# Optimization experiments

Measured on AMD Instinct MI355X. Metric: run time of the kernel, lower is better.

## Reference

```python
import jax, jax.numpy as jnp
import numpy as np

EPS = 1e-12  # F.normalize default eps

def _l1_normalize(x, axis):
    return x / jnp.maximum(jnp.sum(jnp.abs(x), axis=axis, keepdims=True), EPS)


def setup_inputs() -> dict:
    key = jax.random.key(0)
    k1, k2, k3, k4 = jax.random.split(key, 4)
    B_src, S_src, d = 4096, 32, 512
    B_tgt, T = 32, 256
    m = jax.random.normal(k1, (B_src, S_src, d), dtype=jnp.float32)
    om = jax.random.normal(k2, (B_tgt, T, d), dtype=jnp.float32)
    src_mask = jax.random.randint(k3, (B_src, 1, S_src), 0, 2, dtype=jnp.int32)
    tgt_mask = jax.random.randint(k4, (B_tgt, T, T), 0, 2, dtype=jnp.int32)
    return {"m": m, "om": om, "src_mask": src_mask, "tgt_mask": tgt_mask}


def reference(m, om, src_mask, tgt_mask):
    # masked mean readouts (L1-normalized masks as attention weights)
    src_w = _l1_normalize(src_mask.astype(jnp.float32), axis=-1)      # [B_src,1,S_src]
    src_readout = jnp.einsum('bos,bsd->bod', src_w, m)[:, 0, :]       # [B_src,d]
    tgt_w = _l1_normalize(tgt_mask.astype(jnp.float32), axis=-1)      # [B_tgt,T,T]
    tgt_readout = jnp.einsum('btu,bud->btd', tgt_w, om)               # [B_tgt,T,d]

    # pairwise L2 distance over d WITHOUT materializing [B_tgt,T,B_src,d]:
    # ||t - s||^2 = ||t||^2 + ||s||^2 - 2 t.s
    t_sq = jnp.sum(tgt_readout * tgt_readout, axis=-1)                # [B_tgt,T]
    s_sq = jnp.sum(src_readout * src_readout, axis=-1)                # [B_src]
    cross = jnp.einsum('btd,nd->btn', tgt_readout, src_readout)       # [B_tgt,T,B_src]
    d2 = t_sq[..., None] + s_sq[None, None, :] - 2.0 * cross
    dist = jnp.sqrt(jnp.maximum(d2, EPS))
    sim = jnp.exp(-dist)
    sim = _l1_normalize(sim, axis=-1)                                 # [B_tgt,T,B_src]
    return sim
```

## Files before the change

kernel.cpp:

```cpp
#include <hip/hip_runtime.h>
#include <math.h>

#define EPSF 1e-12f

typedef short bf16x8 __attribute__((ext_vector_type(8)));
typedef float f32x4 __attribute__((ext_vector_type(4)));

__device__ __forceinline__ void gload_lds16(const void* g, void* l) {
  __builtin_amdgcn_global_load_lds(
      (const __attribute__((address_space(1))) unsigned int*)g,
      (__attribute__((address_space(3))) unsigned int*)l, 16, 0, 0);
}

__device__ __forceinline__ unsigned short bf16_rne(float f) {
  unsigned int u = __float_as_uint(f);
  u += 0x7fffu + ((u >> 16) & 1u);
  return (unsigned short)(u >> 16);
}

__device__ __forceinline__ float bf16_to_f32(unsigned short h) {
  return __uint_as_float((unsigned int)h << 16);
}

__device__ __forceinline__ float block_reduce_sum_256(float v) {
#pragma unroll
  for (int o = 32; o > 0; o >>= 1) v += __shfl_down(v, o, 64);
  __shared__ float ws4[4];
  const int lane = threadIdx.x & 63;
  const int w = threadIdx.x >> 6;
  if (lane == 0) ws4[w] = v;
  __syncthreads();
  if (threadIdx.x == 0) ws4[0] = ws4[0] + ws4[1] + ws4[2] + ws4[3];
  __syncthreads();
  return ws4[0];
}

__global__ __launch_bounds__(256) void k_src_readout(const float* __restrict__ m,
                                                     const int* __restrict__ src_mask,
                                                     unsigned short* __restrict__ srcRb,
                                                     float* __restrict__ ssq) {
  const int tid = threadIdx.x;
  const int sub = tid >> 7, t = tid & 127;
  const int b = blockIdx.x * 2 + sub;
  __shared__ int msk[2][32];
  __shared__ float sinv[2];
  __shared__ float red[4];
  if (t < 32) msk[sub][t] = src_mask[b * 32 + t];
  __syncthreads();
  if (t == 0) {
    float c = 0.f;
    for (int s = 0; s < 32; ++s) c += (float)msk[sub][s];
    sinv[sub] = 1.0f / fmaxf(c, EPSF);
  }
  __syncthreads();
  const float inv = sinv[sub];
  const float4* mb = (const float4*)(m + (size_t)b * (32 * 512)) + t;
  float ax = 0.f, ay = 0.f, az = 0.f, aw = 0.f;
  for (int s = 0; s < 32; ++s) {
    if (msk[sub][s] != 0) {
      float4 v = mb[s * 128];
      ax += v.x; ay += v.y; az += v.z; aw += v.w;
    }
  }
  ushort4 o;
  o.x = bf16_rne(ax * inv);
  o.y = bf16_rne(ay * inv);
  o.z = bf16_rne(az * inv);
  o.w = bf16_rne(aw * inv);
  *(ushort4*)(srcRb + (size_t)b * 512 + t * 4) = o;
  float fx = bf16_to_f32(o.x), fy = bf16_to_f32(o.y);
  float fz = bf16_to_f32(o.z), fw = bf16_to_f32(o.w);
  float s = fx * fx + fy * fy + fz * fz + fw * fw;
#pragma unroll
  for (int oo = 32; oo > 0; oo >>= 1) s += __shfl_down(s, oo, 64);
  if ((tid & 63) == 0) red[tid >> 6] = s;
  __syncthreads();
  if (t == 0) ssq[b] = red[sub * 2] + red[sub * 2 + 1];
}

#define WST 72
__global__ __launch_bounds__(512) void k_tgt_readout_mfma(
    const float* __restrict__ om, const int* __restrict__ tgt_mask,
    unsigned short* __restrict__ Afrag) {
  const int b = blockIdx.x, dq = blockIdx.y, th = blockIdx.z;
  const int d0 = dq * 128, t0 = th * 128;
  __shared__ unsigned short Wb[128 * WST];
  __shared__ unsigned short omT[128 * WST];
  __shared__ float cntp[128 * 4];
  __shared__ float cnt_inv[128];
  const int tid = threadIdx.x;
  const int lane = tid & 63, w = tid >> 6;
  const int* mbase = tgt_mask + (size_t)b * 65536 + (size_t)t0 * 256;

  {
    const int t = tid >> 2, q = tid & 3;
    const int* mp = mbase + t * 256 + q * 64;
    int c = 0;
#pragma unroll
    for (int k = 0; k < 16; ++k) {
      int4 v = *(const int4*)(mp + 4 * k);
      c += v.x + v.y + v.z + v.w;
    }
    cntp[t * 4 + q] = (float)c;
  }
  __syncthreads();
  if (tid < 128) {
    float c = cntp[tid * 4] + cntp[tid * 4 + 1] + cntp[tid * 4 + 2] + cntp[tid * 4 + 3];
    cnt_inv[tid] = 1.0f / fmaxf(c, EPSF);
  }

  f32x4 acc[8];
#pragma unroll
  for (int di = 0; di < 8; ++di) acc[di] = (f32x4){0.f, 0.f, 0.f, 0.f};

  for (int uc = 0; uc < 4; ++uc) {
    const int ub = uc * 64;
    __syncthreads();
    {
      const int t = tid >> 2, ul0 = (tid & 3) * 16;
      const int* mp = mbase + t * 256 + ub + ul0;
      unsigned short* wp = Wb + t * WST + ul0;
#pragma unroll
      for (int k = 0; k < 4; ++k) {
        int4 v = *(const int4*)(mp + 4 * k);
        ushort4 h;
        h.x = v.x ? 0x3F80 : 0;
        h.y = v.y ? 0x3F80 : 0;
        h.z = v.z ? 0x3F80 : 0;
        h.w = v.w ? 0x3F80 : 0;
        *(ushort4*)(wp + 4 * k) = h;
      }
    }
    {
#pragma unroll
      for (int k = 0; k < 4; ++k) {
        const int idx = tid + 512 * k;
        const int u = idx >> 5, dl = (idx & 31) * 4;
        float4 v = *(const float4*)(om + (size_t)b * 131072 + (size_t)(ub + u) * 512 + d0 + dl);
        omT[(dl + 0) * WST + u] = bf16_rne(v.x);
        omT[(dl + 1) * WST + u] = bf16_rne(v.y);
        omT[(dl + 2) * WST + u] = bf16_rne(v.z);
        omT[(dl + 3) * WST + u] = bf16_rne(v.w);
      }
    }
    __syncthreads();
#pragma unroll
    for (int kt2 = 0; kt2 < 2; ++kt2) {
      const int ko = kt2 * 32 + (lane >> 4) * 8;
      bf16x8 wf = *(const bf16x8*)(Wb + (w * 16 + (lane & 15)) * WST + ko);
      bf16x8 of[8];
#pragma unroll
      for (int di = 0; di < 8; ++di)
        of[di] = *(const bf16x8*)(omT + (di * 16 + (lane & 15)) * WST + ko);
#pragma unroll
      for (int di = 0; di < 8; ++di)
        acc[di] = __builtin_amdgcn_mfma_f32_16x16x32_bf16(of[di], wf, acc[di], 0, 0, 0);
    }
  }

  const int tl = w * 16 + (lane & 15);
  const int rT = b * 256 + t0 + tl;
  const float inv = cnt_inv[tl];
#pragma unroll
  for (int di = 0; di < 8; ++di) {
    const int d = d0 + di * 16 + (lane >> 4) * 4;
    ushort4 o;
    o.x = bf16_rne(acc[di][0] * inv);
    o.y = bf16_rne(acc[di][1] * inv);
    o.z = bf16_rne(acc[di][2] * inv);
    o.w = bf16_rne(acc[di][3] * inv);
    const size_t off =
        (((size_t)(rT >> 4) * 16 + (d >> 5)) * 64 + ((d >> 3) & 3) * 16 + (rT & 15)) * 8 + (d & 7);
    *(ushort4*)(Afrag + off) = o;
  }
}

__global__ __launch_bounds__(256) void k_rowsq_frag(const unsigned short* __restrict__ Afrag,
                                                    float* __restrict__ sq) {
  const int r = blockIdx.x;
  const int tid = threadIdx.x;
  const int g = r >> 4, rl = r & 15;
  const int d = 2 * tid;
  const size_t off = ((size_t)((g * 16 + (d >> 5)) * 64 + ((d >> 3) & 3) * 16 + rl)) * 8 + (d & 7);
  ushort2 v = *(const ushort2*)(Afrag + off);
  float fx = bf16_to_f32(v.x), fy = bf16_to_f32(v.y);
  float s = fx * fx + fy * fy;
  s = block_reduce_sum_256(s);
  if (tid == 0) sq[r] = s;
}

__global__ __launch_bounds__(512, 2) void k_cross_mfma(
    const unsigned short* __restrict__ Afrag, const unsigned short* __restrict__ B,
    const float* __restrict__ tsq, const float* __restrict__ ssq,
    float* __restrict__ out) {
  __shared__ unsigned short Bs[128 * 512];
  const int tid = threadIdx.x;
  const int lane = tid & 63, w = tid >> 6;
  const int bid = blockIdx.x;
  const int xcd = bid & 7, idx = bid >> 3;
  const int row0 = (xcd * 2 + (idx >> 5)) * 512;
  const int col0 = (idx & 31) * 128;
  const int lr = lane & 15, lkh = lane >> 4;

#pragma unroll
  for (int t = 0; t < 16; ++t) {
    const int c = w * 16 + t;
    const int j = c >> 4, kt = c & 15;
    gload_lds16(B + (size_t)(col0 + j * 16 + lr) * 512 + kt * 32 + lkh * 8,
                Bs + (size_t)c * 512);
  }

  f32x4 acc[4][8];
#pragma unroll
  for (int i = 0; i < 4; ++i)
#pragma unroll
    for (int j = 0; j < 8; ++j) acc[i][j] = (f32x4){0.f, 0.f, 0.f, 0.f};

  __syncthreads();

  const unsigned short* ap = Afrag + ((size_t)(row0 >> 4) + w * 4) * (16 * 64 * 8);
#pragma unroll
  for (int kt = 0; kt < 16; ++kt) {
    bf16x8 af[4], bfr[8];
#pragma unroll
    for (int i = 0; i < 4; ++i)
      af[i] = *(const bf16x8*)(ap + (((size_t)i * 16 + kt) * 64 + lane) * 8);
#pragma unroll
    for (int j = 0; j < 8; ++j)
      bfr[j] = *(const bf16x8*)(Bs + ((j * 16 + kt) * 64 + lane) * 8);
#pragma unroll
    for (int i = 0; i < 4; ++i)
#pragma unroll
      for (int j = 0; j < 8; ++j)
        acc[i][j] = __builtin_amdgcn_mfma_f32_16x16x32_bf16(af[i], bfr[j], acc[i][j], 0, 0, 0);
  }

  const int cbase = col0 + (lane & 15);
  const int rbase = row0 + w * 64 + (lane >> 4) * 4;
  float ss[8];
#pragma unroll
  for (int j = 0; j < 8; ++j) ss[j] = ssq[cbase + j * 16];
#pragma unroll
  for (int i = 0; i < 4; ++i) {
#pragma unroll
    for (int r = 0; r < 4; ++r) {
      const int row = rbase + i * 16 + r;
      const float t2 = tsq[row];
      float* op = out + (size_t)row * 4096 + cbase;
#pragma unroll
      for (int j = 0; j < 8; ++j) {
        float d2 = t2 + ss[j] - 2.0f * acc[i][j][r];
        float dist = __builtin_amdgcn_sqrtf(fmaxf(d2, EPSF));
        __builtin_nontemporal_store(__expf(-dist), op + j * 16);
      }
    }
  }
}

__global__ __launch_bounds__(256) void k_norm(float* __restrict__ out) {
  const size_t base = (size_t)blockIdx.x * 4096;
  const int tid = threadIdx.x;
  float4 v[4];
  float s = 0.f;
#pragma unroll
  for (int i = 0; i < 4; ++i) {
    v[i] = *(const float4*)(out + base + (size_t)(tid * 4 + i * 1024));
    s += v[i].x + v[i].y + v[i].z + v[i].w;
  }
  s = block_reduce_sum_256(s);
  const float inv = 1.0f / fmaxf(s, EPSF);
#pragma unroll
  for (int i = 0; i < 4; ++i) {
    f32x4 r;
    r[0] = v[i].x * inv;
    r[1] = v[i].y * inv;
    r[2] = v[i].z * inv;
    r[3] = v[i].w * inv;
    __builtin_nontemporal_store(r, (f32x4*)(out + base + (size_t)(tid * 4 + i * 1024)));
  }
}

extern "C" void kernel_launch(void* const* d_in, const int* in_sizes, int n_in,
                              void* d_out, int out_size, void* d_ws, size_t ws_size,
                              hipStream_t stream) {
  const float* m = (const float*)d_in[0];
  const float* om = (const float*)d_in[1];
  const int* src_mask = (const int*)d_in[2];
  const int* tgt_mask = (const int*)d_in[3];
  float* out = (float*)d_out;

  float* ws = (float*)d_ws;
  float* ssq = ws;
  float* tsq = ssq + 4096;
  unsigned short* srcRb = (unsigned short*)(tsq + 8192);
  unsigned short* Afrag = srcRb + 4096 * 512;

  k_src_readout<<<2048, 256, 0, stream>>>(m, src_mask, srcRb, ssq);
  k_tgt_readout_mfma<<<dim3(32, 4, 2), 512, 0, stream>>>(om, tgt_mask, Afrag);
  k_rowsq_frag<<<8192, 256, 0, stream>>>(Afrag, tsq);
  k_cross_mfma<<<512, 512, 0, stream>>>(Afrag, srcRb, tsq, ssq, out);
  k_norm<<<8192, 256, 0, stream>>>(out);
}
```

Baseline: 159.9 us.

## Store unnormalized similarities as bf16 with fused partial row sums

The cross-distance kernel now writes exp(-dist) into a bf16 intermediate buffer and emits per-tile partial row sums through warp shuffles. A small kernel reduces those partials to inverse row sums, and a scale kernel reads the bf16 values and writes the normalized fp32 output. This halves the intermediate write and read traffic and removes the separate row-sum pass in normalization. In exchange the output carries bf16 rounding error, and the new path only runs if the workspace is large enough, otherwise it falls back to the old fp32 path.

```diff
diff --git a/kernel.cpp b/kernel.cpp
--- a/kernel.cpp
+++ b/kernel.cpp
@@ -189,10 +189,12 @@
   if (tid == 0) sq[r] = s;
 }
 
+template <int BF16SIM>
 __global__ __launch_bounds__(512, 2) void k_cross_mfma(
     const unsigned short* __restrict__ Afrag, const unsigned short* __restrict__ B,
     const float* __restrict__ tsq, const float* __restrict__ ssq,
-    float* __restrict__ out) {
+    unsigned short* __restrict__ simU, float* __restrict__ psum,
+    float* __restrict__ outF) {
   __shared__ unsigned short Bs[128 * 512];
   const int tid = threadIdx.x;
   const int lane = tid & 63, w = tid >> 6;
@@ -246,14 +248,58 @@
     for (int r = 0; r < 4; ++r) {
       const int row = rbase + i * 16 + r;
       const float t2 = tsq[row];
-      float* op = out + (size_t)row * 4096 + cbase;
-#pragma unroll
-      for (int j = 0; j < 8; ++j) {
-        float d2 = t2 + ss[j] - 2.0f * acc[i][j][r];
-        float dist = __builtin_amdgcn_sqrtf(fmaxf(d2, EPSF));
-        __builtin_nontemporal_store(__expf(-dist), op + j * 16);
+      if (BF16SIM) {
+        unsigned short* sp = simU + (size_t)row * 4096 + cbase;
+        float s = 0.f;
+#pragma unroll
+        for (int j = 0; j < 8; ++j) {
+          float d2 = t2 + ss[j] - 2.0f * acc[i][j][r];
+          float sim = __expf(-__builtin_amdgcn_sqrtf(fmaxf(d2, EPSF)));
+          s += sim;
+          __builtin_nontemporal_store(bf16_rne(sim), sp + j * 16);
+        }
+        s += __shfl_xor(s, 1, 64);
+        s += __shfl_xor(s, 2, 64);
+        s += __shfl_xor(s, 4, 64);
+        s += __shfl_xor(s, 8, 64);
+        if ((lane & 15) == 0) psum[(size_t)(col0 >> 7) * 8192 + row] = s;
+      } else {
+        float* op = outF + (size_t)row * 4096 + cbase;
+#pragma unroll
+        for (int j = 0; j < 8; ++j) {
+          float d2 = t2 + ss[j] - 2.0f * acc[i][j][r];
+          float dist = __builtin_amdgcn_sqrtf(fmaxf(d2, EPSF));
+          __builtin_nontemporal_store(__expf(-dist), op + j * 16);
+        }
       }
     }
+  }
+}
+
+__global__ __launch_bounds__(256) void k_sum_reduce(const float* __restrict__ psum,
+                                                    float* __restrict__ rsinv) {
+  const int row = blockIdx.x * 256 + threadIdx.x;
+  float s = 0.f;
+#pragma unroll
+  for (int ct = 0; ct < 32; ++ct) s += psum[(size_t)ct * 8192 + row];
+  rsinv[row] = 1.0f / fmaxf(s, EPSF);
+}
+
+__global__ __launch_bounds__(256) void k_scale(const unsigned short* __restrict__ simU,
+                                               const float* __restrict__ rsinv,
+                                               float* __restrict__ out) {
+  const size_t base = (size_t)blockIdx.x * 4096;
+  const float rsv = rsinv[blockIdx.x];
+  const int tid = threadIdx.x;
+#pragma unroll
+  for (int i = 0; i < 4; ++i) {
+    ushort4 v = *(const ushort4*)(simU + base + (size_t)(tid * 4 + i * 1024));
+    f32x4 r;
+    r[0] = bf16_to_f32(v.x) * rsv;
+    r[1] = bf16_to_f32(v.y) * rsv;
+    r[2] = bf16_to_f32(v.z) * rsv;
+    r[3] = bf16_to_f32(v.w) * rsv;
+    __builtin_nontemporal_store(r, (f32x4*)(out + base + (size_t)(tid * 4 + i * 1024)));
   }
 }
 
@@ -292,12 +338,26 @@
   float* ws = (float*)d_ws;
   float* ssq = ws;
   float* tsq = ssq + 4096;
-  unsigned short* srcRb = (unsigned short*)(tsq + 8192);
+  float* rsinv = tsq + 8192;
+  float* psum = rsinv + 8192;
+  unsigned short* srcRb = (unsigned short*)(psum + 32 * 8192);
   unsigned short* Afrag = srcRb + 4096 * 512;
+  unsigned short* simU = Afrag + (size_t)8192 * 512;
+
+  const size_t need = ((size_t)(4096 + 8192 + 8192) + 32 * 8192) * 4 +
+                      ((size_t)4096 * 512 + (size_t)8192 * 512) * 2 +
+                      (size_t)8192 * 4096 * 2;
+  const bool bf16_path = ws_size >= need;
 
   k_src_readout<<<2048, 256, 0, stream>>>(m, src_mask, srcRb, ssq);
   k_tgt_readout_mfma<<<dim3(32, 4, 2), 512, 0, stream>>>(om, tgt_mask, Afrag);
   k_rowsq_frag<<<8192, 256, 0, stream>>>(Afrag, tsq);
-  k_cross_mfma<<<512, 512, 0, stream>>>(Afrag, srcRb, tsq, ssq, out);
-  k_norm<<<8192, 256, 0, stream>>>(out);
-}
+  if (bf16_path) {
+    k_cross_mfma<1><<<512, 512, 0, stream>>>(Afrag, srcRb, tsq, ssq, simU, psum, out);
+    k_sum_reduce<<<32, 256, 0, stream>>>(psum, rsinv);
+    k_scale<<<8192, 256, 0, stream>>>(simU, rsinv, out);
+  } else {
+    k_cross_mfma<0><<<512, 512, 0, stream>>>(Afrag, srcRb, tsq, ssq, simU, psum, out);
+    k_norm<<<8192, 256, 0, stream>>>(out);
+  }
+}
```

After: 150.8 us. -5.7%, faster.
